# Optimization experiments

Hardware: AMD Instinct MI355X
Metric: run time of the kernel (lower is better)

## Reference

```python
import jax, jax.numpy as jnp
import numpy as np

DM = 1024      # dmodel
HQK = 1024     # heads*dq == heads*dk == heads*dv
FF = 4096
VOCAB = 32000
NCAT = 75
DK = 64        # per-head dk used for 1/sqrt(dk) scaling
UNK_IDX = 1
EPS = 1e-5


def pos_encoding(n, dm):
    pos = jnp.arange(n, dtype=jnp.float32)[:, None]                  # [n,1]
    power = jnp.arange(0, dm, 2, dtype=jnp.float32) / dm             # [dm/2]
    denom = jnp.power(10000.0, power)                                # [dm/2]
    ang = pos / denom                                                # [n,dm/2]
    # even cols = sin, odd cols = cos (interleaved)
    return jnp.stack([jnp.sin(ang), jnp.cos(ang)], axis=-1).reshape(n, dm)


def layernorm(x, g, b):
    mu = jnp.mean(x, axis=-1, keepdims=True)
    var = jnp.var(x, axis=-1, keepdims=True)
    return (x - mu) * jax.lax.rsqrt(var + EPS) * g + b


def setup_inputs() -> dict:
    key = jax.random.key(0)
    ks = jax.random.split(key, 16)
    s = 0.02
    inp = {
        "input_indices": jax.random.randint(ks[0], (8, 2048), 0, VOCAB),
        "emb": jax.random.normal(ks[1], (VOCAB, DM), jnp.float32) * s,
        "Wq": jax.random.normal(ks[2], (DM, HQK), jnp.float32) * s,
        "bq": jnp.zeros((HQK,), jnp.float32),
        "Wk": jax.random.normal(ks[3], (DM, HQK), jnp.float32) * s,
        "bk": jnp.zeros((HQK,), jnp.float32),
        "Wv": jax.random.normal(ks[4], (DM, HQK), jnp.float32) * s,
        "bv": jnp.zeros((HQK,), jnp.float32),
        "Wu": jax.random.normal(ks[5], (HQK, DM), jnp.float32) * s,
        "bu": jnp.zeros((DM,), jnp.float32),
        "g1": jnp.ones((DM,), jnp.float32),
        "be1": jnp.zeros((DM,), jnp.float32),
        "W1": jax.random.normal(ks[6], (DM, FF), jnp.float32) * s,
        "b1": jnp.zeros((FF,), jnp.float32),
        "W2": jax.random.normal(ks[7], (FF, DM), jnp.float32) * s,
        "b2": jnp.zeros((DM,), jnp.float32),
        "g2": jnp.ones((DM,), jnp.float32),
        "be2": jnp.zeros((DM,), jnp.float32),
        "W3": jax.random.normal(ks[8], (DM, DM // 2), jnp.float32) * s,
        "b3": jnp.zeros((DM // 2,), jnp.float32),
        "W4": jax.random.normal(ks[9], (DM // 2, NCAT), jnp.float32) * s,
        "b4": jnp.zeros((NCAT,), jnp.float32),
        "g3": jnp.ones((NCAT,), jnp.float32),
        "be3": jnp.zeros((NCAT,), jnp.float32),
    }
    return inp


def reference(input_indices, emb, Wq, bq, Wk, bk, Wv, bv, Wu, bu, g1, be1,
              W1, b1, W2, b2, g2, be2, W3, b3, W4, b4, g3, be3):
    d, n = input_indices.shape
    idx = jnp.where(input_indices >= VOCAB, UNK_IDX, input_indices)
    x = emb[idx] + pos_encoding(n, DM)[None]                          # [d,n,dm]
    # attention WITHOUT softmax: scores = QK^T/sqrt(dk); attn = scores @ V
    q = x @ Wq + bq
    k = x @ Wk + bk
    v = x @ Wv + bv
    scores = jnp.einsum('bnd,bmd->bnm', q, k) / (DK ** 0.5)           # [d,n,n]
    attn = jnp.einsum('bnm,bmd->bnd', scores, v)                      # [d,n,hdv]
    u = attn @ Wu + bu
    h1 = layernorm(x + u, g1, be1)
    ffo = jax.nn.relu(h1 @ W1 + b1) @ W2 + b2
    h2 = layernorm(h1 + ffo, g2, be2)
    logits = jax.nn.relu(h2 @ W3 + b3) @ W4 + b4                      # [d,n,75]
    return jax.nn.sigmoid(layernorm(logits, g3, be3))
```

## Files before the change

### kernel.cpp

```cpp
#include <hip/hip_runtime.h>
#include <hip/hip_fp16.h>
#include <math.h>

#define DM    1024
#define FFD   4096
#define VOCAB 32000
#define NCAT  75
#define UNK_IDX 1
#define EPS   1e-5f
#define NB    8
#define SEQ   2048
#define T_TOK (NB*SEQ)

using u16   = unsigned short;
using half_t = _Float16;
using half8 = __attribute__((ext_vector_type(8))) _Float16;
using f32x4 = __attribute__((ext_vector_type(4))) float;

struct alignas(8) h4 { half_t s[4]; };

__device__ __forceinline__ void async16(const half_t* g, half_t* l) {
    __builtin_amdgcn_global_load_lds(
        (const __attribute__((address_space(1))) void*)g,
        (__attribute__((address_space(3))) void*)l,
        16, 0, 0);
}

#define VMW(n) asm volatile("s_waitcnt vmcnt(" #n ")" ::: "memory")
#define LGKM0()                                            \
    do {                                                   \
        asm volatile("s_waitcnt lgkmcnt(0)" ::: "memory"); \
        __builtin_amdgcn_sched_barrier(0);                 \
    } while (0)


__global__ __launch_bounds__(256)
void pe_kernel(float* __restrict__ pe)
{
    int gid = blockIdx.x * blockDim.x + threadIdx.x;
    if (gid >= SEQ * DM) return;
    int dcol = gid & (DM - 1);
    int t    = gid >> 10;
    int p = dcol >> 1;
    float power = (float)p / 512.0f;
    float denom = powf(10000.0f, power);
    float ang = (float)t / denom;
    pe[gid] = (dcol & 1) ? cosf(ang) : sinf(ang);
}

__global__ __launch_bounds__(256)
void embed_pos_kernel(const int* __restrict__ idx,
                      const float* __restrict__ emb,
                      const float* __restrict__ pe,
                      float* __restrict__ xf, half_t* __restrict__ xh)
{
    int gid4 = blockIdx.x * blockDim.x + threadIdx.x;
    if (gid4 >= T_TOK * DM / 4) return;
    int tok = gid4 >> 8;
    int c4  = (gid4 & 255) << 2;
    int t   = tok & (SEQ - 1);
    int id = idx[tok];
    if (id >= VOCAB || id < 0) id = UNK_IDX;
    float4 e = *(const float4*)(emb + (long long)id * DM + c4);
    float4 q = *(const float4*)(pe + (long long)t * DM + c4);
    float4 v = make_float4(e.x + q.x, e.y + q.y, e.z + q.z, e.w + q.w);
    *(float4*)(xf + (long long)tok * DM + c4) = v;
    h4 pk = {{(half_t)v.x, (half_t)v.y, (half_t)v.z, (half_t)v.w}};
    *(h4*)(xh + (long long)tok * DM + c4) = pk;
}

__global__ __launch_bounds__(256)
void transpose_h_kernel(const float* __restrict__ in, half_t* __restrict__ out,
                        int K, int N, int Npad)
{
    __shared__ float t[32][33];
    int n0 = blockIdx.x * 32, k0 = blockIdx.y * 32;
    int tx = threadIdx.x & 31, ty = threadIdx.x >> 5;
#pragma unroll
    for (int i = 0; i < 4; i++) {
        int k = k0 + ty + i * 8, n = n0 + tx;
        t[ty + i * 8][tx] = (k < K && n < N) ? in[(long long)k * N + n] : 0.f;
    }
    __syncthreads();
#pragma unroll
    for (int i = 0; i < 4; i++) {
        int n = n0 + ty + i * 8, k = k0 + tx;
        if (n < Npad && k < K)
            out[(long long)n * K + k] = (half_t)t[tx][ty + i * 8];
    }
}

__global__ __launch_bounds__(128)
void pad_bias_kernel(const float* __restrict__ b, float* __restrict__ bp)
{
    int i = threadIdx.x;
    bp[i] = (i < NCAT) ? b[i] : 0.f;
}

template<int OUT_MODE>
__global__ __launch_bounds__(256)
void gemm_nt(const half_t* __restrict__ A, const half_t* __restrict__ B,
             const float* __restrict__ bias, const float* __restrict__ resid,
             void* __restrict__ Cout,
             int M, int N, int K, int ld,
             long long sA, long long sB, long long sC,
             float scale, int do_relu)
{
    A += (long long)blockIdx.z * sA;
    B += (long long)blockIdx.z * sB;
    const int tid  = threadIdx.x;
    const int lane = tid & 63;
    const int w    = tid >> 6;
    const int wm   = w >> 1, wn = w & 1;
    const long long row0 = (long long)blockIdx.y * 128;
    const long long col0 = (long long)blockIdx.x * 128;

    __shared__ half_t smem[4 * 4096];
    half_t* const As = smem;
    half_t* const Bs = smem + 2 * 4096;

    f32x4 acc[4][4];
    const f32x4 zero = {0.f, 0.f, 0.f, 0.f};
#pragma unroll
    for (int i = 0; i < 4; i++)
#pragma unroll
        for (int j = 0; j < 4; j++) acc[i][j] = zero;

    const int ldrow = lane & 15;
    const int swcol = (lane >> 4) << 3;
    const int l8    = lane << 3;

    const int KT = K / 32;

#define ISSUE(k0, buf)                                                         \
    {                                                                          \
        _Pragma("unroll")                                                      \
        for (int it = 0; it < 2; ++it) {                                       \
            int rb = (it * 4 + w) * 16;                                        \
            long long ao = (row0 + rb + ldrow) * (long long)ld + (k0) + swcol; \
            long long bo = (col0 + rb + ldrow) * (long long)ld + (k0) + swcol; \
            async16(A + ao, As + (buf) * 4096 + rb * 32);                      \
            async16(B + bo, Bs + (buf) * 4096 + rb * 32);                      \
        }                                                                      \
    }

    ISSUE(0, 0);
    for (int kt = 0; kt < KT; ++kt) {
        const int cur = kt & 1;
        __syncthreads();
        if (kt + 1 < KT) ISSUE((kt + 1) * 32, cur ^ 1);

        half8 af[4], bf[4];
#pragma unroll
        for (int i = 0; i < 4; ++i)
            af[i] = *(const half8*)(As + cur * 4096 + (wm * 4 + i) * 512 + l8);
#pragma unroll
        for (int j = 0; j < 4; ++j)
            bf[j] = *(const half8*)(Bs + cur * 4096 + (wn * 4 + j) * 512 + l8);
#pragma unroll
        for (int i = 0; i < 4; ++i)
#pragma unroll
            for (int j = 0; j < 4; ++j)
                acc[i][j] = __builtin_amdgcn_mfma_f32_16x16x32_f16(
                    af[i], bf[j], acc[i][j], 0, 0, 0);
    }
#undef ISSUE

    float* ls = (float*)smem;
    const int ldp = 132;
    const int qr = (lane >> 4) * 4;
    const int lc = lane & 15;
    float bvj[4];
#pragma unroll
    for (int j = 0; j < 4; ++j)
        bvj[j] = bias ? bias[col0 + wn * 64 + j * 16 + lc] : 0.f;
    const float* rz = (OUT_MODE == 0 && resid) ? resid + (long long)blockIdx.z * sC : nullptr;

#pragma unroll
    for (int i = 0; i < 4; ++i) {
        __syncthreads();
#pragma unroll
        for (int j = 0; j < 4; ++j) {
            int col = wn * 64 + j * 16 + lc;
#pragma unroll
            for (int r = 0; r < 4; ++r) {
                float f = acc[i][j][r] * scale + bvj[j];
                if (do_relu) f = fmaxf(f, 0.f);
                ls[(wm * 16 + qr + r) * ldp + col] = f;
            }
        }
        __syncthreads();
        if (OUT_MODE == 2) {
#pragma unroll
            for (int rep = 0; rep < 4; ++rep) {
                int idx = rep * 256 + tid;
                int n   = idx >> 3;
                int k   = idx & 7;
                int lr0 = k * 4;
                h4 pk;
                long long arow0 = (lr0 < 16 ? 0 : 48) + i * 16 + lr0;
#pragma unroll
                for (int r = 0; r < 4; ++r)
                    pk.s[r] = (half_t)ls[(lr0 + r) * ldp + n];
                long long gr = row0 + arow0;
                int b  = (int)(gr >> 11);
                int tl = (int)(gr & (SEQ - 1));
                half_t* C = (half_t*)Cout;
                *(h4*)(C + (long long)b * N * SEQ + (col0 + n) * SEQ + tl) = pk;
            }
        } else {
#pragma unroll
            for (int rep = 0; rep < 4; ++rep) {
                int idx = rep * 256 + tid;
                int lr  = idx >> 5;
                int c4  = (idx & 31) << 2;
                long long arow = (lr < 16 ? 0 : 48) + i * 16 + lr;
                float4 v = *(float4*)&ls[lr * ldp + c4];
                long long base = (row0 + arow) * N + col0 + c4;
                if (OUT_MODE == 0) {
                    float* C = (float*)Cout + blockIdx.z * sC;
                    if (rz) {
                        float4 x = *(const float4*)(rz + base);
                        v.x += x.x; v.y += x.y; v.z += x.z; v.w += x.w;
                    }
                    *(float4*)(C + base) = v;
                } else {
                    half_t* C = (half_t*)Cout + blockIdx.z * sC;
                    h4 pk = {{(half_t)v.x, (half_t)v.y, (half_t)v.z, (half_t)v.w}};
                    *(h4*)(C + base) = pk;
                }
            }
        }
    }
}

template<int OUT_MODE>
__global__ __launch_bounds__(512, 2)
void gemm256(const half_t* __restrict__ A, const half_t* __restrict__ B,
             const float* __restrict__ bias, const float* __restrict__ resid,
             void* __restrict__ Cout,
             int N, int K, int ld,
             long long sA, long long sB, long long sC,
             long long sKA, long long sKB, long long sKC, int ksh,
             float scale, int do_relu)
{
    const int kz       = (int)(blockIdx.z & ((1u << ksh) - 1u));
    const long long zb = (long long)(blockIdx.z >> ksh);
    A += zb * sA + (long long)kz * sKA;
    B += zb * sB + (long long)kz * sKB;

    int bx = blockIdx.x, by = blockIdx.y;
    const int nxy = gridDim.x * gridDim.y;
    if ((nxy & 7) == 0) {
        const int orig = by * gridDim.x + bx;
        const int cpx  = nxy >> 3;
        const int wg   = (orig & 7) * cpx + (orig >> 3);
        bx = wg % gridDim.x;
        by = wg / gridDim.x;
    }
    const long long row0 = (long long)by * 256;
    const long long col0 = (long long)bx * 256;

    const int tid  = threadIdx.x;
    const int lane = tid & 63;
    const int w    = tid >> 6;
    const int wm   = w >> 2, wn = w & 3;
    const int l8   = lane << 3;

    __shared__ half_t smem[65536];
    half_t* const As = smem;
    half_t* const Bs = smem + 32768;

    f32x4 acc[8][4];
    const f32x4 zero = {0.f, 0.f, 0.f, 0.f};
#pragma unroll
    for (int i = 0; i < 8; i++)
#pragma unroll
        for (int j = 0; j < 4; j++) acc[i][j] = zero;

    const int srow = w * 16 + (lane & 15);
    const int scol = (lane >> 4) << 3;

#define STAGE(G, plane, rb, kb)                                                   \
    {                                                                             \
        _Pragma("unroll")                                                         \
        for (int it_ = 0; it_ < 2; ++it_) {                                       \
            async16((G) + ((rb) + it_ * 128 + srow) * (long long)ld + (kb) + scol,\
                    (plane) + it_ * 4096 + w * 512);                              \
        }                                                                         \
    }
#define RDA(base_, rg0_)                                                          \
    _Pragma("unroll")                                                             \
    for (int q_ = 0; q_ < 4; ++q_)                                                \
        af[q_] = *(const half8*)((base_) + ((rg0_) + q_) * 512 + l8);
#define RDB(base_)                                                                \
    _Pragma("unroll")                                                             \
    for (int q_ = 0; q_ < 4; ++q_)                                                \
        bf[q_] = *(const half8*)((base_) + (wn * 4 + q_) * 512 + l8);
#define MM16(o_)                                                                  \
    _Pragma("unroll")                                                             \
    for (int mi_ = 0; mi_ < 4; ++mi_)                                             \
    _Pragma("unroll")                                                             \
    for (int ni_ = 0; ni_ < 4; ++ni_)                                             \
        acc[(o_) + mi_][ni_] = __builtin_amdgcn_mfma_f32_16x16x32_f16(            \
            af[mi_], bf[ni_], acc[(o_) + mi_][ni_], 0, 0, 0);
#define MFMA_PHASE(o_)                                      \
    __builtin_amdgcn_s_barrier();                           \
    LGKM0();                                                \
    __builtin_amdgcn_s_setprio(1);                          \
    MM16(o_);                                               \
    __builtin_amdgcn_s_setprio(0);                          \
    __builtin_amdgcn_s_barrier();

    const int KT = K >> 6;

    STAGE(A, As,        row0, 0);
    STAGE(B, Bs,        col0, 0);
    STAGE(A, As + 8192, row0, 32);
    STAGE(B, Bs + 8192, col0, 32);
    VMW(4);
    __builtin_amdgcn_s_barrier();

    half8 af[4], bf[4];
    for (int t = 0; t < KT; ++t) {
        const int db = (t & 1) << 14;
        const int nb = 16384 - db;
        const half_t* Ap0 = As + db;
        const half_t* Ap1 = As + db + 8192;
        const half_t* Bp0 = Bs + db;
        const half_t* Bp1 = Bs + db + 8192;
        const int kn = (t + 1 < KT ? t + 1 : t) << 6;

        RDA(Ap0, wm * 8); RDB(Bp0);
        STAGE(A, As + nb, row0, kn);
        MFMA_PHASE(0);
        RDA(Ap0, wm * 8 + 4);
        STAGE(B, Bs + nb, col0, kn);
        VMW(4);
        MFMA_PHASE(4);
        RDA(Ap1, wm * 8); RDB(Bp1);
        STAGE(A, As + nb + 8192, row0, kn + 32);
        MFMA_PHASE(0);
        RDA(Ap1, wm * 8 + 4);
        STAGE(B, Bs + nb + 8192, col0, kn + 32);
        VMW(4);
        MFMA_PHASE(4);
    }
#undef STAGE
#undef RDA
#undef RDB
#undef MM16
#undef MFMA_PHASE

    VMW(0);
    __syncthreads();
    float* const ls = (float*)smem;
    const int ldp = 268;
    const int qr = (lane >> 4) * 4;
    const int lc = lane & 15;
    float bvn[4];
#pragma unroll
    for (int ni = 0; ni < 4; ++ni)
        bvn[ni] = bias ? bias[col0 + wn * 64 + ni * 16 + lc] : 0.f;
    const float* rz = (OUT_MODE == 0 && resid) ? resid + zb * sC : nullptr;

#pragma unroll
    for (int i = 0; i < 4; ++i) {
        if (i) __syncthreads();
#pragma unroll
        for (int h = 0; h < 2; ++h) {
            const int mi = 2 * i + h;
#pragma unroll
            for (int ni = 0; ni < 4; ++ni) {
#pragma unroll
                for (int r = 0; r < 4; ++r) {
                    float f = acc[mi][ni][r] * scale + bvn[ni];
                    if (do_relu) f = fmaxf(f, 0.f);
                    ls[(wm * 32 + h * 16 + qr + r) * ldp + wn * 64 + ni * 16 + lc] = f;
                }
            }
        }
        __syncthreads();
#pragma unroll
        for (int rep = 0; rep < 8; ++rep) {
            int idx2 = rep * 512 + tid;
            int r  = idx2 >> 6;
            int c4 = (idx2 & 63) << 2;
            long long grow = row0 + (r < 32 ? i * 32 + r : 128 + i * 32 + (r - 32));
            long long base = grow * N + col0 + c4;
            float4 v = *(float4*)&ls[r * ldp + c4];
            if (OUT_MODE == 0) {
                float* C = (float*)Cout + zb * sC + (long long)kz * sKC;
                if (rz) {
                    float4 x = *(const float4*)(rz + base);
                    v.x += x.x; v.y += x.y; v.z += x.z; v.w += x.w;
                }
                *(float4*)(C + base) = v;
            } else {
                half_t* C = (half_t*)Cout + zb * sC;
                h4 pk = {{(half_t)v.x, (half_t)v.y, (half_t)v.z, (half_t)v.w}};
                *(h4*)(C + base) = pk;
            }
        }
    }
}

__global__ __launch_bounds__(256)
void add_ln_kernel(const float* __restrict__ X, const float* __restrict__ Y,
                   const float* __restrict__ Z, const float* __restrict__ cb,
                   const float* __restrict__ g, const float* __restrict__ b,
                   float* __restrict__ outf, half_t* __restrict__ outh)
{
    int row = blockIdx.x;
    int tid = threadIdx.x;
    float4 v = ((const float4*)(X + (long long)row * DM))[tid];
    if (Y) {
        float4 y = ((const float4*)(Y + (long long)row * DM))[tid];
        v.x += y.x; v.y += y.y; v.z += y.z; v.w += y.w;
    }
    if (Z) {
        float4 z = ((const float4*)(Z + (long long)row * DM))[tid];
        v.x += z.x; v.y += z.y; v.z += z.z; v.w += z.w;
    }
    if (cb) {
        float4 c = ((const float4*)cb)[tid];
        v.x += c.x; v.y += c.y; v.z += c.z; v.w += c.w;
    }
    float s  = v.x + v.y + v.z + v.w;
    float s2 = v.x * v.x + v.y * v.y + v.z * v.z + v.w * v.w;
#pragma unroll
    for (int o = 1; o < 64; o <<= 1) {
        s  += __shfl_xor(s,  o, 64);
        s2 += __shfl_xor(s2, o, 64);
    }
    __shared__ float rs[4], rs2[4], stats[2];
    int wid = tid >> 6;
    if ((tid & 63) == 0) { rs[wid] = s; rs2[wid] = s2; }
    __syncthreads();
    if (tid == 0) {
        float S  = rs[0] + rs[1] + rs[2] + rs[3];
        float S2 = rs2[0] + rs2[1] + rs2[2] + rs2[3];
        float mean = S / (float)DM;
        float var  = S2 / (float)DM - mean * mean;
        stats[0] = mean;
        stats[1] = rsqrtf(var + EPS);
    }
    __syncthreads();
    float mean = stats[0], rstd = stats[1];
    float4 gg = ((const float4*)g)[tid];
    float4 bb = ((const float4*)b)[tid];
    float4 o;
    o.x = (v.x - mean) * rstd * gg.x + bb.x;
    o.y = (v.y - mean) * rstd * gg.y + bb.y;
    o.z = (v.z - mean) * rstd * gg.z + bb.z;
    o.w = (v.w - mean) * rstd * gg.w + bb.w;
    if (outf) ((float4*)(outf + (long long)row * DM))[tid] = o;
    h4 pk = {{(half_t)o.x, (half_t)o.y, (half_t)o.z, (half_t)o.w}};
    *(h4*)(outh + (long long)row * DM + tid * 4) = pk;
}

__global__ __launch_bounds__(64)
void ln75_sigmoid_kernel(const float* __restrict__ L,
                         const float* __restrict__ g, const float* __restrict__ b,
                         float* __restrict__ out)
{
    int row = blockIdx.x;
    int t   = threadIdx.x;
    const float* lr = L + (long long)row * 128;
    float e0 = (t < NCAT) ? lr[t] : 0.f;
    float e1 = (t + 64 < NCAT) ? lr[t + 64] : 0.f;
    float s  = e0 + e1;
    float s2 = e0 * e0 + e1 * e1;
#pragma unroll
    for (int o = 1; o < 64; o <<= 1) {
        s  += __shfl_xor(s,  o, 64);
        s2 += __shfl_xor(s2, o, 64);
    }
    float mean = s / (float)NCAT;
    float var  = s2 / (float)NCAT - mean * mean;
    float rstd = rsqrtf(var + EPS);
    if (t < NCAT) {
        float z = (e0 - mean) * rstd * g[t] + b[t];
        out[(long long)row * NCAT + t] = 1.f / (1.f + expf(-z));
    }
    if (t + 64 < NCAT) {
        float z = (e1 - mean) * rstd * g[t + 64] + b[t + 64];
        out[(long long)row * NCAT + t + 64] = 1.f / (1.f + expf(-z));
    }
}

extern "C" void kernel_launch(void* const* d_in, const int* in_sizes, int n_in,
                              void* d_out, int out_size, void* d_ws, size_t ws_size,
                              hipStream_t stream)
{
    const int*   idx = (const int*)  d_in[0];
    const float* emb = (const float*)d_in[1];
    const float* Wq  = (const float*)d_in[2];
    const float* bq  = (const float*)d_in[3];
    const float* Wk  = (const float*)d_in[4];
    const float* bk  = (const float*)d_in[5];
    const float* Wv  = (const float*)d_in[6];
    const float* bv  = (const float*)d_in[7];
    const float* Wu  = (const float*)d_in[8];
    const float* bu  = (const float*)d_in[9];
    const float* g1  = (const float*)d_in[10];
    const float* be1 = (const float*)d_in[11];
    const float* W1  = (const float*)d_in[12];
    const float* b1  = (const float*)d_in[13];
    const float* W2  = (const float*)d_in[14];
    const float* b2  = (const float*)d_in[15];
    const float* g2  = (const float*)d_in[16];
    const float* be2 = (const float*)d_in[17];
    const float* W3  = (const float*)d_in[18];
    const float* b3  = (const float*)d_in[19];
    const float* W4  = (const float*)d_in[20];
    const float* b4  = (const float*)d_in[21];
    const float* g3  = (const float*)d_in[22];
    const float* be3 = (const float*)d_in[23];

    const long long TD  = (long long)T_TOK * DM;
    char* p = (char*)d_ws;
    char* R_A = p; p += TD * 4;
    char* R_B = p; p += TD * 2;
    char* R_C = p; p += TD * 2;
    char* R_D = p; p += TD * 2;
    char* R_D2 = p; p += TD * 2;
    char* R_E = p; p += TD * 4;
    char* R_F = p; p += (long long)NB * DM * DM * 4;
    char* R_G = p; p += (long long)T_TOK * 128 * 4;
    float* pe = (float*)p; p += (long long)SEQ * DM * 4;
    half_t* Wqh = (half_t*)p; p += DM*DM*2;
    half_t* Wkh = (half_t*)p; p += DM*DM*2;
    half_t* Wvh = (half_t*)p; p += DM*DM*2;
    half_t* Wuh = (half_t*)p; p += DM*DM*2;
    half_t* W1h = (half_t*)p; p += (long long)FFD*DM*2;
    half_t* W2h = (half_t*)p; p += (long long)DM*FFD*2;
    half_t* W3h = (half_t*)p; p += 512*DM*2;
    half_t* W4h = (half_t*)p; p += 128*512*2;
    float*  b4p = (float*)p;  p += 128*4;

    float*  Xf   = (float*)R_A;
    float*  Pff  = (float*)R_A;
    half_t* Xh   = (half_t*)R_B;
    half_t* h2h  = (half_t*)R_B;
    half_t* Qh   = (half_t*)R_C;
    half_t* h1h  = (half_t*)R_C;
    half_t* Kt   = (half_t*)R_D;
    half_t* Vt   = (half_t*)R_D2;
    half_t* f1h  = (half_t*)R_D;
    float*  usum = (float*)R_E;
    float*  h1f  = (float*)R_E;
    half_t* ktv2 = (half_t*)R_F;
    half_t* M2t  = (half_t*)(R_F + (long long)NB*DM*DM*2);
    half_t* l1h  = (half_t*)R_F;
    float*  LOG  = (float*)R_G;
    float*  out  = (float*)d_out;

    dim3 blk(256);
    dim3 blk5(512);

    transpose_h_kernel<<<dim3(32, 32),  blk, 0, stream>>>(Wq, Wqh, DM, DM, DM);
    transpose_h_kernel<<<dim3(32, 32),  blk, 0, stream>>>(Wk, Wkh, DM, DM, DM);
    transpose_h_kernel<<<dim3(32, 32),  blk, 0, stream>>>(Wv, Wvh, DM, DM, DM);
    transpose_h_kernel<<<dim3(32, 32),  blk, 0, stream>>>(Wu, Wuh, DM, DM, DM);
    transpose_h_kernel<<<dim3(128, 32), blk, 0, stream>>>(W1, W1h, DM, FFD, FFD);
    transpose_h_kernel<<<dim3(32, 128), blk, 0, stream>>>(W2, W2h, FFD, DM, DM);
    transpose_h_kernel<<<dim3(16, 32),  blk, 0, stream>>>(W3, W3h, DM, 512, 512);
    transpose_h_kernel<<<dim3(4, 16),   blk, 0, stream>>>(W4, W4h, 512, NCAT, 128);
    pad_bias_kernel<<<1, 128, 0, stream>>>(b4, b4p);
    pe_kernel<<<(SEQ * DM + 255) / 256, blk, 0, stream>>>(pe);

    embed_pos_kernel<<<(T_TOK * DM / 4 + 255) / 256, blk, 0, stream>>>(idx, emb, pe, Xf, Xh);

    gemm256<1><<<dim3(4, 64, 1), blk5, 0, stream>>>(Xh, Wqh, bq, nullptr, Qh,
        DM, DM, DM, 0, 0, 0, 0, 0, 0, 0, 1.f, 0);
    gemm_nt<2><<<dim3(8, 128, 1), blk, 0, stream>>>(Xh, Wkh, bk, nullptr, Kt,
        T_TOK, DM, DM, DM, 0, 0, 0, 1.f, 0);
    gemm_nt<2><<<dim3(8, 128, 1), blk, 0, stream>>>(Xh, Wvh, bv, nullptr, Vt,
        T_TOK, DM, DM, DM, 0, 0, 0, 1.f, 0);

    gemm_nt<1><<<dim3(8, 8, NB), blk, 0, stream>>>(Kt, Vt, nullptr, nullptr, ktv2,
        DM, DM, SEQ, SEQ, (long long)DM * SEQ, (long long)DM * SEQ, (long long)DM * DM,
        0.125f, 0);

    gemm_nt<1><<<dim3(8, 8, NB), blk, 0, stream>>>(Wuh, ktv2, nullptr, nullptr, M2t,
        DM, DM, DM, DM, 0, (long long)DM * DM, (long long)DM * DM, 1.f, 0);

    gemm256<0><<<dim3(4, 8, NB), blk5, 0, stream>>>(Qh, M2t, bu, Xf, usum,
        DM, DM, DM, (long long)SEQ * DM, (long long)DM * DM, (long long)SEQ * DM,
        0, 0, 0, 0, 1.f, 0);

    add_ln_kernel<<<T_TOK, blk, 0, stream>>>(usum, nullptr, nullptr, nullptr,
                                             g1, be1, h1f, h1h);

    for (int c = 0; c < 2; c++) {
        const half_t* h1c = h1h + (long long)c * 8192 * DM;
        gemm256<1><<<dim3(16, 32, 1), blk5, 0, stream>>>(h1c, W1h, b1, nullptr, f1h,
            FFD, DM, DM, 0, 0, 0, 0, 0, 0, 0, 1.f, 1);
        gemm256<0><<<dim3(4, 32, 2), blk5, 0, stream>>>(f1h, W2h, nullptr, nullptr, Pff,
            DM, 2048, FFD, 0, 0, 0,
            2048, 2048, (long long)8192 * DM, 1, 1.f, 0);
        add_ln_kernel<<<8192, blk, 0, stream>>>(h1f + (long long)c * 8192 * DM,
            Pff, Pff + (long long)8192 * DM, b2, g2, be2,
            nullptr, h2h + (long long)c * 8192 * DM);
    }

    gemm_nt<1><<<dim3(4, 128, 1), blk, 0, stream>>>(h2h, W3h, b3, nullptr, l1h,
        T_TOK, 512, DM, DM, 0, 0, 0, 1.f, 1);
    gemm_nt<0><<<dim3(1, 128, 1), blk, 0, stream>>>(l1h, W4h, b4p, nullptr, LOG,
        T_TOK, 128, 512, 512, 0, 0, 0, 1.f, 0);

    ln75_sigmoid_kernel<<<T_TOK, 64, 0, stream>>>(LOG, g3, be3, out);
}
```

Baseline: 1.121 ms.

## Restructure GEMM main loop with ping-pong fragment registers and fewer barriers

The GEMM K-loop now issues all four async global-to-LDS stages for the next tile at the start of each iteration. It uses two sets of A/B fragment registers so LDS reads for the next MFMA cluster overlap the current one. Partial lgkmcnt waits replace the full waits, and barriers per iteration drop from eight to two. The aim is to cut synchronisation stalls and hide LDS latency, at the cost of more vector registers, which may lower occupancy.

```diff
diff --git a/kernel.cpp b/kernel.cpp
--- a/kernel.cpp
+++ b/kernel.cpp
@@ -27,11 +27,12 @@
 }
 
 #define VMW(n) asm volatile("s_waitcnt vmcnt(" #n ")" ::: "memory")
-#define LGKM0()                                            \
-    do {                                                   \
-        asm volatile("s_waitcnt lgkmcnt(0)" ::: "memory"); \
-        __builtin_amdgcn_sched_barrier(0);                 \
+#define LGKMC(n)                                               \
+    do {                                                       \
+        asm volatile("s_waitcnt lgkmcnt(" #n ")" ::: "memory");\
+        __builtin_amdgcn_sched_barrier(0);                     \
     } while (0)
+#define SCHED_FENCE() __builtin_amdgcn_sched_barrier(0)
 
 
 __global__ __launch_bounds__(256)
@@ -289,28 +290,26 @@
                     (plane) + it_ * 4096 + w * 512);                              \
         }                                                                         \
     }
-#define RDA(base_, rg0_)                                                          \
+#define RDA(dst_, base_, rg0_)                                                    \
     _Pragma("unroll")                                                             \
     for (int q_ = 0; q_ < 4; ++q_)                                                \
-        af[q_] = *(const half8*)((base_) + ((rg0_) + q_) * 512 + l8);
-#define RDB(base_)                                                                \
+        dst_[q_] = *(const half8*)((base_) + ((rg0_) + q_) * 512 + l8);
+#define RDB(dst_, base_)                                                          \
     _Pragma("unroll")                                                             \
     for (int q_ = 0; q_ < 4; ++q_)                                                \
-        bf[q_] = *(const half8*)((base_) + (wn * 4 + q_) * 512 + l8);
-#define MM16(o_)                                                                  \
+        dst_[q_] = *(const half8*)((base_) + (wn * 4 + q_) * 512 + l8);
+#define MM16(o_, AF, BF)                                                          \
     _Pragma("unroll")                                                             \
     for (int mi_ = 0; mi_ < 4; ++mi_)                                             \
     _Pragma("unroll")                                                             \
     for (int ni_ = 0; ni_ < 4; ++ni_)                                             \
         acc[(o_) + mi_][ni_] = __builtin_amdgcn_mfma_f32_16x16x32_f16(            \
-            af[mi_], bf[ni_], acc[(o_) + mi_][ni_], 0, 0, 0);
-#define MFMA_PHASE(o_)                                      \
-    __builtin_amdgcn_s_barrier();                           \
-    LGKM0();                                                \
+            AF[mi_], BF[ni_], acc[(o_) + mi_][ni_], 0, 0, 0);
+#define CLUSTER(o_, AF, BF)                                 \
     __builtin_amdgcn_s_setprio(1);                          \
-    MM16(o_);                                               \
+    MM16(o_, AF, BF);                                       \
     __builtin_amdgcn_s_setprio(0);                          \
-    __builtin_amdgcn_s_barrier();
+    SCHED_FENCE();
 
     const int KT = K >> 6;
 
@@ -318,10 +317,8 @@
     STAGE(B, Bs,        col0, 0);
     STAGE(A, As + 8192, row0, 32);
     STAGE(B, Bs + 8192, col0, 32);
-    VMW(4);
-    __builtin_amdgcn_s_barrier();
-
-    half8 af[4], bf[4];
+
+    half8 afP[4], afQ[4], bfP[4], bfQ[4];
     for (int t = 0; t < KT; ++t) {
         const int db = (t & 1) << 14;
         const int nb = 16384 - db;
@@ -331,26 +328,32 @@
         const half_t* Bp1 = Bs + db + 8192;
         const int kn = (t + 1 < KT ? t + 1 : t) << 6;
 
-        RDA(Ap0, wm * 8); RDB(Bp0);
-        STAGE(A, As + nb, row0, kn);
-        MFMA_PHASE(0);
-        RDA(Ap0, wm * 8 + 4);
-        STAGE(B, Bs + nb, col0, kn);
-        VMW(4);
-        MFMA_PHASE(4);
-        RDA(Ap1, wm * 8); RDB(Bp1);
+        STAGE(A, As + nb,        row0, kn);
+        STAGE(B, Bs + nb,        col0, kn);
         STAGE(A, As + nb + 8192, row0, kn + 32);
-        MFMA_PHASE(0);
-        RDA(Ap1, wm * 8 + 4);
         STAGE(B, Bs + nb + 8192, col0, kn + 32);
-        VMW(4);
-        MFMA_PHASE(4);
+        VMW(8);
+        __builtin_amdgcn_s_barrier();
+
+        RDA(afP, Ap0, wm * 8);  RDB(bfP, Bp0);
+        RDA(afQ, Ap0, wm * 8 + 4);
+        LGKMC(4);
+        CLUSTER(0, afP, bfP);
+        RDA(afP, Ap1, wm * 8);  RDB(bfQ, Bp1);
+        LGKMC(8);
+        CLUSTER(4, afQ, bfP);
+        RDA(afQ, Ap1, wm * 8 + 4);
+        LGKMC(4);
+        CLUSTER(0, afP, bfQ);
+        LGKMC(0);
+        CLUSTER(4, afQ, bfQ);
+        __builtin_amdgcn_s_barrier();
     }
 #undef STAGE
 #undef RDA
 #undef RDB
 #undef MM16
-#undef MFMA_PHASE
+#undef CLUSTER
 
     VMW(0);
     __syncthreads();
```

After: 1.193 ms. +6.4%, slower.
